# Optimization experiments

Measured on AMD Instinct MI355X. Metric: run time of the kernel, lower is better.

## Reference

```python
import jax, jax.numpy as jnp
import numpy as np

# Hard-coded constants from the original module
GAMMA = 0.1      # self.gamma default
N_STEPS = 10     # self.n_steps default
RHO = 0.9        # RMSProp decay
LR = 0.009       # RMSProp learning rate
MOM = 0.9        # momentum
EPS = 1e-8       # RMSProp epsilon
ABS_EPS = 1e-6   # diff_abs smoothing: diff_abs(x) = sqrt(x^2 + 1e-6)

B, IN_DIM, OUT_DIM = 4096, 2048, 4096


def setup_inputs() -> dict:
    key = jax.random.key(0)
    k1, k2 = jax.random.split(key)
    inputs = jax.random.normal(k1, (B, IN_DIM), dtype=jnp.float32)
    # keras 'uniform' init: U(-0.05, 0.05), shape (output_dim, input_dim)
    W = jax.random.uniform(k2, (OUT_DIM, IN_DIM), minval=-0.05, maxval=0.05, dtype=jnp.float32)
    return {"inputs": inputs, "W": W}


def reference(inputs, W):
    batch = inputs.shape[0]
    out_dim = W.shape[0]
    a = jnp.sqrt(inputs * inputs + ABS_EPS)          # diff_abs(inputs), [B, in_dim]
    act = lambda u: 0.5 * (1.0 + jnp.exp(-u))        # self.activation

    def cost(x):
        # l1_norm.sum() + l1_inov + own_norm  (prior = 0)
        l1 = (GAMMA * act(x @ W) * a).sum()
        l1_inov = (GAMMA / 10.0) * jnp.sum(x * x)
        own = GAMMA * jnp.sum(jnp.sqrt(x * x + ABS_EPS))
        return l1 + l1_inov + own

    grad_cost = jax.grad(cost)

    def step(carry, _):
        x, acc1, acc2 = carry
        g = grad_cost(x)                              # [B, out_dim]
        new_acc1 = RHO * acc1 + (1.0 - RHO) * g * g
        denom = jnp.sqrt(new_acc1 + EPS)
        new_acc2 = MOM * acc2 - LR * g / denom
        cand = x - LR * g / denom
        t = 0.1 * LR / denom                          # elementwise prox threshold
        new_x = jnp.maximum(cand - t, 0.0) + jnp.minimum(cand + t, 0.0) + MOM * new_acc2
        new_x = jax.lax.stop_gradient(new_x)          # theano disconnected_grad
        return (new_x, new_acc1, new_acc2), None

    z = jnp.zeros((batch, out_dim), dtype=inputs.dtype)
    # scan runs n_steps; last step's l1_norm uses the state after n_steps-1 updates,
    # so run n_steps-1 updates then compute the final l1_norm directly.
    (x, _, _), _ = jax.lax.scan(step, (z, z, z), None, length=N_STEPS - 1)
    return GAMMA * act(x @ W) * a                     # outputs[-1][-1]: last l1_norm, [B, in_dim]
```

## Files before the change

### kernel.cpp

```cpp
#include <hip/hip_runtime.h>
#include <cstdint>
#include <cstddef>

#define B_DIM   4096
#define IN_DIM  2048
#define OUT_DIM 4096

typedef __attribute__((ext_vector_type(8))) __bf16 bf16x8;
typedef __attribute__((ext_vector_type(4))) float  f32x4;
typedef unsigned short ushortT;

__device__ __forceinline__ ushortT f2bf(float f) {
    unsigned int u = __float_as_uint(f);
    u += 0x7FFFu + ((u >> 16) & 1u);
    return (ushortT)(u >> 16);
}
__device__ __forceinline__ float bf2f(ushortT b) {
    return __uint_as_float(((unsigned int)b) << 16);
}

__device__ __forceinline__ void gload16(const void* g, void* l) {
    __builtin_amdgcn_global_load_lds(
        (const __attribute__((address_space(1))) void*)g,
        (__attribute__((address_space(3))) void*)l, 16, 0, 0);
}

__global__ void prep_g0_kernel(const float* __restrict__ in, ushortT* __restrict__ Gb) {
    int i = blockIdx.x * 256 + threadIdx.x;
    float4 v = reinterpret_cast<const float4*>(in)[i];
    ushort4 g;
    g.x = f2bf(-0.05f * sqrtf(v.x * v.x + 1e-6f));
    g.y = f2bf(-0.05f * sqrtf(v.y * v.y + 1e-6f));
    g.z = f2bf(-0.05f * sqrtf(v.z * v.z + 1e-6f));
    g.w = f2bf(-0.05f * sqrtf(v.w * v.w + 1e-6f));
    reinterpret_cast<ushort4*>(Gb)[i] = g;
}

__global__ void conv_w_kernel(const float* __restrict__ W, ushortT* __restrict__ Wb,
                              ushortT* __restrict__ WTb) {
    __shared__ float tile[64][65];
    const int i0 = blockIdx.x * 64;
    const int j0 = blockIdx.y * 64;
    const int c  = threadIdx.x & 63;
    const int rq = threadIdx.x >> 6;
#pragma unroll
    for (int rp = 0; rp < 16; ++rp) {
        int row = rp * 4 + rq;
        float w = W[(size_t)(j0 + row) * IN_DIM + i0 + c];
        tile[row][c] = w;
        Wb[(size_t)(j0 + row) * IN_DIM + i0 + c] = f2bf(w);
    }
    __syncthreads();
#pragma unroll
    for (int rp = 0; rp < 16; ++rp) {
        int row = rp * 4 + rq;
        WTb[(size_t)(i0 + row) * OUT_DIM + j0 + c] = f2bf(tile[c][row]);
    }
}

template <int EPI, int BM>
__global__ __launch_bounds__(512, 1)
void gemm_ring(const ushortT* __restrict__ A, const ushortT* __restrict__ Bm,
               int N, int K,
               const float* __restrict__ inb, ushortT* __restrict__ Gb,
               float* __restrict__ out,
               ushortT* __restrict__ acc1, ushortT* __restrict__ acc2,
               ushortT* __restrict__ xb) {
    constexpr int BN   = 256;
    constexpr int ASZ  = BM * 64;
    constexpr int BSZ  = BN * 64;
    constexpr int SLOT = ASZ + BSZ;
    constexpr int LA   = BM / 128;
    constexpr int LB   = BN / 128;
    constexpr int L    = LA + LB;
    constexpr int MR   = BM / 32;
    __shared__ alignas(16) char smem[4 * SLOT];

    const int tid  = threadIdx.x;
    const int lane = tid & 63;
    const int w    = tid >> 6;
    const int wm   = w >> 2;
    const int wn   = w & 3;
    const int nbx  = N / BN;
    const int nwg  = gridDim.x;
    const int cpx  = nwg >> 3;
    const int bid  = (int)blockIdx.x;
    const int swz  = (bid & 7) * cpx + (bid >> 3);
    const int bx   = swz % nbx;
    const int by   = swz / nbx;
    const int row0 = by * BM;
    const int col0 = bx * BN;

    const size_t strideK2 = (size_t)K * 2;

    const char* gAp[LA]; int lAo[LA];
#pragma unroll
    for (int i = 0; i < LA; ++i) {
        int Lp  = i * 512 + tid;
        int row = Lp >> 2, sl = Lp & 3;
        int src = sl ^ ((row >> 1) & 3);
        gAp[i] = (const char*)A + (size_t)(row0 + row) * strideK2 + src * 16;
        lAo[i] = i * 8192 + w * 1024;
    }
    const char* gBp[LB]; int lBo[LB];
#pragma unroll
    for (int i = 0; i < LB; ++i) {
        int Lp  = i * 512 + tid;
        int row = Lp >> 2, sl = Lp & 3;
        int src = sl ^ ((row >> 1) & 3);
        gBp[i] = (const char*)Bm + (size_t)(col0 + row) * strideK2 + src * 16;
        lBo[i] = ASZ + i * 8192 + w * 1024;
    }
    auto stage = [&](int tt) {
        char* sb = smem + (tt & 3) * SLOT;
        const size_t kb = (size_t)tt * 64;
#pragma unroll
        for (int i = 0; i < LA; ++i) gload16(gAp[i] + kb, sb + lAo[i]);
#pragma unroll
        for (int i = 0; i < LB; ++i) gload16(gBp[i] + kb, sb + lBo[i]);
    };

    int aRd[MR], bRd[4];
#pragma unroll
    for (int m = 0; m < MR; ++m) {
        int row = wm * (BM / 2) + m * 16 + (lane & 15);
        aRd[m] = row * 64 + (((lane >> 4) ^ ((row >> 1) & 3)) * 16);
    }
#pragma unroll
    for (int n = 0; n < 4; ++n) {
        int row = wn * 64 + n * 16 + (lane & 15);
        bRd[n] = ASZ + row * 64 + (((lane >> 4) ^ ((row >> 1) & 3)) * 16);
    }

    f32x4 acc[MR][4] = {};
    const int nt = K >> 5;

    stage(0); stage(1); stage(2);
    asm volatile("s_waitcnt vmcnt(%0)" :: "n"(2 * L) : "memory");
    __builtin_amdgcn_s_barrier();
    bf16x8 FA[8], FB[8];
#pragma unroll
    for (int m = 0; m < 4; ++m) FA[m]     = *reinterpret_cast<const bf16x8*>(smem + aRd[m]);
#pragma unroll
    for (int n = 0; n < 4; ++n) FA[4 + n] = *reinterpret_cast<const bf16x8*>(smem + bRd[n]);

    auto iter = [&](int t, bf16x8 (&cur)[8], bf16x8 (&nxt)[8]) {
        if (t + 3 < nt) stage(t + 3);
        const int rem = nt - 1 - t;
        if (rem >= 3)      asm volatile("s_waitcnt vmcnt(%0)" :: "n"(2 * L) : "memory");
        else if (rem == 2) asm volatile("s_waitcnt vmcnt(%0)" :: "n"(L)     : "memory");
        else               asm volatile("s_waitcnt vmcnt(0)"  ::: "memory");
        __builtin_amdgcn_s_barrier();
        __builtin_amdgcn_sched_barrier(0);
        const char* sbC = smem + (t & 3) * SLOT;
        const char* sbN = smem + ((t + 1) & 3) * SLOT;
        bf16x8 a2[4];
        if constexpr (MR == 8) {
#pragma unroll
            for (int m = 0; m < 4; ++m) a2[m] = *reinterpret_cast<const bf16x8*>(sbC + aRd[m + 4]);
        }
        if (rem >= 1) {
#pragma unroll
            for (int m = 0; m < 4; ++m) nxt[m]     = *reinterpret_cast<const bf16x8*>(sbN + aRd[m]);
#pragma unroll
            for (int n = 0; n < 4; ++n) nxt[4 + n] = *reinterpret_cast<const bf16x8*>(sbN + bRd[n]);
        }
        __builtin_amdgcn_sched_barrier(0);
        __builtin_amdgcn_s_setprio(1);
#pragma unroll
        for (int m = 0; m < 4; ++m)
#pragma unroll
            for (int n = 0; n < 4; ++n)
                acc[m][n] = __builtin_amdgcn_mfma_f32_16x16x32_bf16(cur[m], cur[4 + n], acc[m][n], 0, 0, 0);
        if constexpr (MR == 8) {
#pragma unroll
            for (int m = 0; m < 4; ++m)
#pragma unroll
                for (int n = 0; n < 4; ++n)
                    acc[m + 4][n] = __builtin_amdgcn_mfma_f32_16x16x32_bf16(a2[m], cur[4 + n], acc[m + 4][n], 0, 0, 0);
        }
        __builtin_amdgcn_s_setprio(0);
        __builtin_amdgcn_s_barrier();
        __builtin_amdgcn_sched_barrier(0);
    };

    for (int t = 0; t < nt; t += 2) {
        iter(t,     FA, FB);
        iter(t + 1, FB, FA);
    }

    float* lep = (float*)(smem + w * 4352);
    const int li = lane >> 4;
    const int lc = lane & 15;
    const int row0w = row0 + wm * (BM / 2);
    const int col0w = col0 + wn * 64;
#pragma unroll
    for (int m = 0; m < MR; ++m) {
#pragma unroll
        for (int n = 0; n < 4; ++n)
#pragma unroll
            for (int i = 0; i < 4; ++i)
                lep[(li * 4 + i) * 68 + n * 16 + lc] = acc[m][n][i];
        asm volatile("s_waitcnt lgkmcnt(0)" ::: "memory");
        __builtin_amdgcn_sched_barrier(0);
#pragma unroll
        for (int rr = 0; rr < 4; ++rr) {
            const int row = rr + li * 4;
            float4 v = *reinterpret_cast<const float4*>(&lep[row * 68 + lc * 4]);
            const size_t idx  = (size_t)(row0w + m * 16 + row) * N + col0w + lc * 4;
            const size_t idx4 = idx >> 2;
            if constexpr (EPI == 0) {
                float4 iv = reinterpret_cast<const float4*>(inb)[idx4];
                ushort4 g;
                g.x = f2bf(-0.05f * sqrtf(iv.x * iv.x + 1e-6f) * expf(-v.x));
                g.y = f2bf(-0.05f * sqrtf(iv.y * iv.y + 1e-6f) * expf(-v.y));
                g.z = f2bf(-0.05f * sqrtf(iv.z * iv.z + 1e-6f) * expf(-v.z));
                g.w = f2bf(-0.05f * sqrtf(iv.w * iv.w + 1e-6f) * expf(-v.w));
                *reinterpret_cast<ushort4*>(&Gb[idx]) = g;
            } else if constexpr (EPI == 1) {
                float4 iv = reinterpret_cast<const float4*>(inb)[idx4];
                float4 o;
                o.x = 0.05f * (1.0f + expf(-v.x)) * sqrtf(iv.x * iv.x + 1e-6f);
                o.y = 0.05f * (1.0f + expf(-v.y)) * sqrtf(iv.y * iv.y + 1e-6f);
                o.z = 0.05f * (1.0f + expf(-v.z)) * sqrtf(iv.z * iv.z + 1e-6f);
                o.w = 0.05f * (1.0f + expf(-v.w)) * sqrtf(iv.w * iv.w + 1e-6f);
                reinterpret_cast<float4*>(out)[idx4] = o;
            } else {
                ushort4 xu  = *reinterpret_cast<const ushort4*>(&xb[idx]);
                ushort4 a1u = *reinterpret_cast<const ushort4*>(&acc1[idx]);
                ushort4 a2u = *reinterpret_cast<const ushort4*>(&acc2[idx]);
                float xs[4] = {bf2f(xu.x), bf2f(xu.y), bf2f(xu.z), bf2f(xu.w)};
                float vs[4] = {v.x, v.y, v.z, v.w};
                ushortT a1s[4] = {a1u.x, a1u.y, a1u.z, a1u.w};
                ushortT a2s[4] = {a2u.x, a2u.y, a2u.z, a2u.w};
                ushortT a1n[4], a2n[4], xbn[4];
#pragma unroll
                for (int j = 0; j < 4; ++j) {
                    float g    = vs[j] + 0.02f * xs[j] + 0.1f * xs[j] * rsqrtf(xs[j] * xs[j] + 1e-6f);
                    float a1   = 0.9f * bf2f(a1s[j]) + 0.1f * g * g;
                    float inv  = rsqrtf(a1 + 1e-8f);
                    float r_   = 0.009f * g * inv;
                    float a2   = 0.9f * bf2f(a2s[j]) - r_;
                    float cand = xs[j] - r_;
                    float t_   = 0.0009f * inv;
                    float xn   = fmaxf(cand - t_, 0.0f) + fminf(cand + t_, 0.0f) + 0.9f * a2;
                    a1n[j] = f2bf(a1); a2n[j] = f2bf(a2); xbn[j] = f2bf(xn);
                }
                *reinterpret_cast<ushort4*>(&acc1[idx]) = make_ushort4(a1n[0], a1n[1], a1n[2], a1n[3]);
                *reinterpret_cast<ushort4*>(&acc2[idx]) = make_ushort4(a2n[0], a2n[1], a2n[2], a2n[3]);
                *reinterpret_cast<ushort4*>(&xb[idx])   = make_ushort4(xbn[0], xbn[1], xbn[2], xbn[3]);
            }
        }
        asm volatile("s_waitcnt lgkmcnt(0)" ::: "memory");
    }
}

extern "C" void kernel_launch(void* const* d_in, const int* in_sizes, int n_in,
                              void* d_out, int out_size, void* d_ws, size_t ws_size,
                              hipStream_t stream) {
    const float* in = (const float*)d_in[0];
    const float* W  = (const float*)d_in[1];
    float* out = (float*)d_out;
    char* ws = (char*)d_ws;

    ushortT* acc1 = (ushortT*)(ws);
    ushortT* acc2 = (ushortT*)(ws + ((size_t)32  << 20));
    ushortT* xb   = (ushortT*)(ws + ((size_t)64  << 20));
    ushortT* Wb   = (ushortT*)(ws + ((size_t)96  << 20));
    ushortT* WTb  = (ushortT*)(ws + ((size_t)112 << 20));
    ushortT* Gb   = (ushortT*)(ws + ((size_t)128 << 20));

    hipMemsetAsync(ws, 0, (size_t)96 << 20, stream);

    prep_g0_kernel<<<dim3(B_DIM * IN_DIM / 4 / 256), dim3(256), 0, stream>>>(in, Gb);
    conv_w_kernel<<<dim3(IN_DIM / 64, OUT_DIM / 64), dim3(256), 0, stream>>>(W, Wb, WTb);

    for (int step = 0; step < 9; ++step) {
        if (step > 0) {
            gemm_ring<0, 128><<<dim3(256), dim3(512), 0, stream>>>(
                xb, WTb, IN_DIM, OUT_DIM, in, Gb, nullptr, nullptr, nullptr, nullptr);
        }
        gemm_ring<2, 256><<<dim3(256), dim3(512), 0, stream>>>(
            Gb, Wb, OUT_DIM, IN_DIM, nullptr, nullptr, nullptr, acc1, acc2, xb);
    }
    gemm_ring<1, 128><<<dim3(256), dim3(512), 0, stream>>>(
        xb, WTb, IN_DIM, OUT_DIM, in, nullptr, out, nullptr, nullptr, nullptr);
}
```

Measured before the change: 1.619 ms.

## Restructure GEMM main loop into phased two-tile steps with interleaved chunk loads

Replaces the register double-buffered per-tile loop with a loop that handles two K-tiles per outer iteration. Each iteration is split into MR small phases, and each phase reads an A fragment pair straight from LDS, issues a slice of the global-to-LDS loads for tiles t+3 and t+4, and then runs 8 MFMAs. Spreading the prefetch across phases is meant to smooth memory issue and cut register use from the FA/FB fragment buffers. In exchange it adds a barrier and an lgkmcnt(0) wait per phase, which exposes LDS read latency with no register prefetch to hide it.

```diff
diff --git a/kernel.cpp b/kernel.cpp
--- a/kernel.cpp
+++ b/kernel.cpp
@@ -60,12 +60,12 @@
 
 template <int EPI, int BM>
 __global__ __launch_bounds__(512, 1)
-void gemm_ring(const ushortT* __restrict__ A, const ushortT* __restrict__ Bm,
-               int N, int K,
-               const float* __restrict__ inb, ushortT* __restrict__ Gb,
-               float* __restrict__ out,
-               ushortT* __restrict__ acc1, ushortT* __restrict__ acc2,
-               ushortT* __restrict__ xb) {
+void gemm_phase(const ushortT* __restrict__ A, const ushortT* __restrict__ Bm,
+                int N, int K,
+                const float* __restrict__ inb, ushortT* __restrict__ Gb,
+                float* __restrict__ out,
+                ushortT* __restrict__ acc1, ushortT* __restrict__ acc2,
+                ushortT* __restrict__ xb) {
     constexpr int BN   = 256;
     constexpr int ASZ  = BM * 64;
     constexpr int BSZ  = BN * 64;
@@ -74,6 +74,7 @@
     constexpr int LB   = BN / 128;
     constexpr int L    = LA + LB;
     constexpr int MR   = BM / 32;
+    constexpr int HP   = MR / 2;
     __shared__ alignas(16) char smem[4 * SLOT];
 
     const int tid  = threadIdx.x;
@@ -93,31 +94,31 @@
 
     const size_t strideK2 = (size_t)K * 2;
 
-    const char* gAp[LA]; int lAo[LA];
+    const char* gp[L]; int lo[L];
 #pragma unroll
     for (int i = 0; i < LA; ++i) {
         int Lp  = i * 512 + tid;
         int row = Lp >> 2, sl = Lp & 3;
         int src = sl ^ ((row >> 1) & 3);
-        gAp[i] = (const char*)A + (size_t)(row0 + row) * strideK2 + src * 16;
-        lAo[i] = i * 8192 + w * 1024;
-    }
-    const char* gBp[LB]; int lBo[LB];
+        gp[i] = (const char*)A + (size_t)(row0 + row) * strideK2 + src * 16;
+        lo[i] = i * 8192 + w * 1024;
+    }
 #pragma unroll
     for (int i = 0; i < LB; ++i) {
         int Lp  = i * 512 + tid;
         int row = Lp >> 2, sl = Lp & 3;
         int src = sl ^ ((row >> 1) & 3);
-        gBp[i] = (const char*)Bm + (size_t)(col0 + row) * strideK2 + src * 16;
-        lBo[i] = ASZ + i * 8192 + w * 1024;
-    }
-    auto stage = [&](int tt) {
+        gp[LA + i] = (const char*)Bm + (size_t)(col0 + row) * strideK2 + src * 16;
+        lo[LA + i] = ASZ + i * 8192 + w * 1024;
+    }
+    auto stage_all = [&](int tt) {
         char* sb = smem + (tt & 3) * SLOT;
         const size_t kb = (size_t)tt * 64;
 #pragma unroll
-        for (int i = 0; i < LA; ++i) gload16(gAp[i] + kb, sb + lAo[i]);
-#pragma unroll
-        for (int i = 0; i < LB; ++i) gload16(gBp[i] + kb, sb + lBo[i]);
+        for (int c = 0; c < L; ++c) gload16(gp[c] + kb, sb + lo[c]);
+    };
+    auto stage_chunk = [&](int tt, int c) {
+        gload16(gp[c] + (size_t)tt * 64, smem + (tt & 3) * SLOT + lo[c]);
     };
 
     int aRd[MR], bRd[4];
@@ -135,59 +136,50 @@
     f32x4 acc[MR][4] = {};
     const int nt = K >> 5;
 
-    stage(0); stage(1); stage(2);
-    asm volatile("s_waitcnt vmcnt(%0)" :: "n"(2 * L) : "memory");
-    __builtin_amdgcn_s_barrier();
-    bf16x8 FA[8], FB[8];
-#pragma unroll
-    for (int m = 0; m < 4; ++m) FA[m]     = *reinterpret_cast<const bf16x8*>(smem + aRd[m]);
-#pragma unroll
-    for (int n = 0; n < 4; ++n) FA[4 + n] = *reinterpret_cast<const bf16x8*>(smem + bRd[n]);
-
-    auto iter = [&](int t, bf16x8 (&cur)[8], bf16x8 (&nxt)[8]) {
-        if (t + 3 < nt) stage(t + 3);
-        const int rem = nt - 1 - t;
-        if (rem >= 3)      asm volatile("s_waitcnt vmcnt(%0)" :: "n"(2 * L) : "memory");
-        else if (rem == 2) asm volatile("s_waitcnt vmcnt(%0)" :: "n"(L)     : "memory");
-        else               asm volatile("s_waitcnt vmcnt(0)"  ::: "memory");
+    stage_all(0); stage_all(1); stage_all(2);
+
+    for (int tt = 0; tt < nt; tt += 2) {
+        if (tt + 2 < nt) asm volatile("s_waitcnt vmcnt(%0)" :: "n"(L) : "memory");
+        else             asm volatile("s_waitcnt vmcnt(0)"  ::: "memory");
         __builtin_amdgcn_s_barrier();
         __builtin_amdgcn_sched_barrier(0);
-        const char* sbC = smem + (t & 3) * SLOT;
-        const char* sbN = smem + ((t + 1) & 3) * SLOT;
-        bf16x8 a2[4];
-        if constexpr (MR == 8) {
-#pragma unroll
-            for (int m = 0; m < 4; ++m) a2[m] = *reinterpret_cast<const bf16x8*>(sbC + aRd[m + 4]);
+
+        bf16x8 bF[4];
+#pragma unroll
+        for (int p = 0; p < MR; ++p) {
+            constexpr int C0 = 1, C1 = 1;
+            const int sslot = p / HP;
+            const int mp    = p % HP;
+            const char* sb  = smem + ((tt + sslot) & 3) * SLOT;
+            if (mp == 0) {
+#pragma unroll
+                for (int n = 0; n < 4; ++n)
+                    bF[n] = *reinterpret_cast<const bf16x8*>(sb + bRd[n]);
+            }
+            bf16x8 aF0 = *reinterpret_cast<const bf16x8*>(sb + aRd[2 * mp]);
+            bf16x8 aF1 = *reinterpret_cast<const bf16x8*>(sb + aRd[2 * mp + 1]);
+#pragma unroll
+            for (int c = p * 2 * L / MR; c < (p + 1) * 2 * L / MR; ++c) {
+                const int tile = (c < L) ? (tt + 3) : (tt + 4);
+                const int cc   = (c < L) ? c : c - L;
+                if (tile < nt) stage_chunk(tile, cc);
+            }
+            asm volatile("s_waitcnt lgkmcnt(0)" ::: "memory");
+            __builtin_amdgcn_sched_barrier(0);
+            __builtin_amdgcn_s_setprio(1);
+#pragma unroll
+            for (int n = 0; n < 4; ++n)
+                acc[2 * mp][n] = __builtin_amdgcn_mfma_f32_16x16x32_bf16(aF0, bF[n], acc[2 * mp][n], 0, 0, 0);
+#pragma unroll
+            for (int n = 0; n < 4; ++n)
+                acc[2 * mp + 1][n] = __builtin_amdgcn_mfma_f32_16x16x32_bf16(aF1, bF[n], acc[2 * mp + 1][n], 0, 0, 0);
+            __builtin_amdgcn_s_setprio(0);
+            __builtin_amdgcn_s_barrier();
+            __builtin_amdgcn_sched_barrier(0);
         }
-        if (rem >= 1) {
-#pragma unroll
-            for (int m = 0; m < 4; ++m) nxt[m]     = *reinterpret_cast<const bf16x8*>(sbN + aRd[m]);
-#pragma unroll
-            for (int n = 0; n < 4; ++n) nxt[4 + n] = *reinterpret_cast<const bf16x8*>(sbN + bRd[n]);
-        }
-        __builtin_amdgcn_sched_barrier(0);
-        __builtin_amdgcn_s_setprio(1);
-#pragma unroll
-        for (int m = 0; m < 4; ++m)
-#pragma unroll
-            for (int n = 0; n < 4; ++n)
-                acc[m][n] = __builtin_amdgcn_mfma_f32_16x16x32_bf16(cur[m], cur[4 + n], acc[m][n], 0, 0, 0);
-        if constexpr (MR == 8) {
-#pragma unroll
-            for (int m = 0; m < 4; ++m)
-#pragma unroll
-                for (int n = 0; n < 4; ++n)
-                    acc[m + 4][n] = __builtin_amdgcn_mfma_f32_16x16x32_bf16(a2[m], cur[4 + n], acc[m + 4][n], 0, 0, 0);
-        }
-        __builtin_amdgcn_s_setprio(0);
-        __builtin_amdgcn_s_barrier();
-        __builtin_amdgcn_sched_barrier(0);
-    };
-
-    for (int t = 0; t < nt; t += 2) {
-        iter(t,     FA, FB);
-        iter(t + 1, FB, FA);
-    }
+    }
+
+    __builtin_amdgcn_s_barrier();
 
     float* lep = (float*)(smem + w * 4352);
     const int li = lane >> 4;
@@ -277,12 +269,12 @@
 
     for (int step = 0; step < 9; ++step) {
         if (step > 0) {
-            gemm_ring<0, 128><<<dim3(256), dim3(512), 0, stream>>>(
+            gemm_phase<0, 128><<<dim3(256), dim3(512), 0, stream>>>(
                 xb, WTb, IN_DIM, OUT_DIM, in, Gb, nullptr, nullptr, nullptr, nullptr);
         }
-        gemm_ring<2, 256><<<dim3(256), dim3(512), 0, stream>>>(
+        gemm_phase<2, 256><<<dim3(256), dim3(512), 0, stream>>>(
             Gb, Wb, OUT_DIM, IN_DIM, nullptr, nullptr, nullptr, acc1, acc2, xb);
     }
-    gemm_ring<1, 128><<<dim3(256), dim3(512), 0, stream>>>(
+    gemm_phase<1, 128><<<dim3(256), dim3(512), 0, stream>>>(
         xb, WTb, IN_DIM, OUT_DIM, in, nullptr, out, nullptr, nullptr, nullptr);
 }
```

After: 1.560 ms. 1.04x faster.
